# Optimization experiments

Measured on AMD Instinct MI355X. Metric: run time of the kernel, lower is better.

## Reference

```python
import jax, jax.numpy as jnp
import numpy as np
import math

B, T, C = 8, 2048, 1024
H = 16
HD = C // H  # 64 head dim; RoPE operates on HD//2 complex pairs


def setup_inputs() -> dict:
    key = jax.random.key(0)
    k1, k2, k3, k4 = jax.random.split(key, 4)
    x = jax.random.normal(k1, (B, T, C), dtype=jnp.float32)
    # RoPE angles theta[t, i] = t * base**(-2i/HD), as in standard precompute_freqs_cis
    inv_freq = 1.0 / (10000.0 ** (jnp.arange(0, HD, 2, dtype=jnp.float32) / HD))
    freqs = jnp.arange(T, dtype=jnp.float32)[:, None] * inv_freq[None, :]  # [T, HD//2]
    W_attn = jax.random.normal(k2, (C, 3 * C), dtype=jnp.float32) * 0.02
    b_attn = jnp.zeros((3 * C,), dtype=jnp.float32)
    W_proj = jax.random.normal(k3, (C, C), dtype=jnp.float32) * 0.02
    b_proj = jnp.zeros((C,), dtype=jnp.float32)
    return {"x": x, "freqs": freqs, "W_attn": W_attn, "b_attn": b_attn,
            "W_proj": W_proj, "b_proj": b_proj}


def _apply_rope(t, cos, sin):
    # t: [B, T, H, HD] -> view as complex pairs on last dim
    tr = t.reshape(*t.shape[:-1], HD // 2, 2)
    t0, t1 = tr[..., 0], tr[..., 1]
    out0 = t0 * cos - t1 * sin
    out1 = t0 * sin + t1 * cos
    return jnp.stack([out0, out1], axis=-1).reshape(t.shape)


def reference(x, freqs, W_attn, b_attn, W_proj, b_proj):
    Bx, Tx, Cx = x.shape
    qkv = x @ W_attn + b_attn                      # [B, T, 3C]
    q, k, v = jnp.split(qkv, 3, axis=2)
    q = q.reshape(Bx, Tx, H, HD)
    k = k.reshape(Bx, Tx, H, HD)
    v = v.reshape(Bx, Tx, H, HD)
    # rotary embedding (freqs broadcast over batch and heads)
    cos = jnp.cos(freqs)[None, :, None, :]        # [1, T, 1, HD//2]
    sin = jnp.sin(freqs)[None, :, None, :]
    q = _apply_rope(q, cos, sin)
    k = _apply_rope(k, cos, sin)
    # [B, H, T, HD]
    q = q.transpose(0, 2, 1, 3)
    k = k.transpose(0, 2, 1, 3)
    v = v.transpose(0, 2, 1, 3)
    scale = 1.0 / math.sqrt(HD)
    scores = jnp.einsum('bhqd,bhkd->bhqk', q, k) * scale
    causal = jnp.tril(jnp.ones((Tx, Tx), dtype=bool))
    scores = jnp.where(causal[None, None], scores, jnp.finfo(scores.dtype).min)
    att = jax.nn.softmax(scores, axis=-1)
    y = jnp.einsum('bhqk,bhkd->bhqd', att, v)     # [B, H, T, HD]
    y = y.transpose(0, 2, 1, 3).reshape(Bx, Tx, Cx)
    y = y @ W_proj + b_proj
    return y
```

## Files before the change

kernel.cpp:

```cpp
#include <hip/hip_runtime.h>

#define B_ 8
#define T_ 2048
#define C_ 1024
#define H_ 16
#define HD_ 64
#define BH_ (B_ * H_)
#define M_ (B_ * T_)

typedef __attribute__((ext_vector_type(8))) short short8;
typedef __attribute__((ext_vector_type(4))) float floatx4;
typedef __attribute__((ext_vector_type(16))) float floatx16;

__device__ __forceinline__ short f2bf(float f) {
  unsigned int u = __float_as_uint(f);
  u += 0x7fffu + ((u >> 16) & 1u);
  return (short)(u >> 16);
}

__device__ __forceinline__ unsigned cvtpk(float a, float b) {
  unsigned r;
  asm("v_cvt_pk_bf16_f32 %0, %1, %2" : "=v"(r) : "v"(a), "v"(b));
  return r;
}

__device__ __forceinline__ float ex2(float x) {
  float r;
  asm("v_exp_f32 %0, %1" : "=v"(r) : "v"(x));
  return r;
}

__device__ __forceinline__ void g2lds16(const void* g, void* l) {
  __builtin_amdgcn_global_load_lds(
      (const __attribute__((address_space(1))) unsigned int*)g,
      (__attribute__((address_space(3))) unsigned int*)l, 16, 0, 0);
}

__global__ void cvt_x_kernel(const float* __restrict__ x, short* __restrict__ xb, int n8) {
  int i = blockIdx.x * 256 + threadIdx.x;
  if (i >= n8) return;
  const float4* p = reinterpret_cast<const float4*>(x) + (size_t)i * 2;
  float4 a = p[0], b = p[1];
  short8 o;
  o[0] = f2bf(a.x); o[1] = f2bf(a.y); o[2] = f2bf(a.z); o[3] = f2bf(a.w);
  o[4] = f2bf(b.x); o[5] = f2bf(b.y); o[6] = f2bf(b.z); o[7] = f2bf(b.w);
  reinterpret_cast<short8*>(xb)[i] = o;
}

__global__ void transpose_w_kernel(const float* __restrict__ W, short* __restrict__ Wt,
                                   int K, int N) {
  __shared__ float tile[64][65];
  const int k0 = blockIdx.y * 64;
  const int n0 = blockIdx.x * 64;
  const int tid = threadIdx.x;
  const int cc = tid & 15, rr = tid >> 4;
#pragma unroll
  for (int p = 0; p < 4; ++p) {
    int r = p * 16 + rr;
    float4 v = *reinterpret_cast<const float4*>(&W[(size_t)(k0 + r) * N + n0 + cc * 4]);
    tile[r][cc * 4 + 0] = v.x; tile[r][cc * 4 + 1] = v.y;
    tile[r][cc * 4 + 2] = v.z; tile[r][cc * 4 + 3] = v.w;
  }
  __syncthreads();
  const int kk8 = tid & 7, nn = tid >> 3;
#pragma unroll
  for (int p = 0; p < 2; ++p) {
    int n = p * 32 + nn;
    short8 o;
#pragma unroll
    for (int j = 0; j < 8; ++j) o[j] = f2bf(tile[kk8 * 8 + j][n]);
    *reinterpret_cast<short8*>(&Wt[(size_t)(n0 + n) * K + k0 + kk8 * 8]) = o;
  }
}

__global__ void trig_kernel(const float* __restrict__ freqs, float2* __restrict__ cs, int n) {
  int i = blockIdx.x * 256 + threadIdx.x;
  if (i < n) {
    float f = freqs[i];
    cs[i] = make_float2(cosf(f), sinf(f));
  }
}

#define WAIT8 asm volatile("s_waitcnt vmcnt(8)" ::: "memory")
#define WAIT6 asm volatile("s_waitcnt vmcnt(6)" ::: "memory")
#define WAIT4 asm volatile("s_waitcnt vmcnt(4)" ::: "memory")
#define WAIT2 asm volatile("s_waitcnt vmcnt(2)" ::: "memory")
#define WAIT0 asm volatile("s_waitcnt vmcnt(0)" ::: "memory")

#define GITER(T, CUR, NXT)                                                        \
  {                                                                               \
    const int tbR = ((T) & 3) << 15;                                              \
                                     \
    _Pragma("unroll") for (int i = 0; i < 4; ++i)                                 \
        af1[i] = *reinterpret_cast<const short8*>(ldsb + tbR + aoff[4 + i]);      \
    __builtin_amdgcn_s_setprio(1);                                                \
    _Pragma("unroll") for (int m = 0; m < 4; ++m)                                 \
        _Pragma("unroll") for (int n = 0; n < 4; ++n)                             \
            acc[m][n] = __builtin_amdgcn_mfma_f32_16x16x32_bf16(                  \
                af0[m], CUR[n], acc[m][n], 0, 0, 0);                              \
    __builtin_amdgcn_s_setprio(0);                                                \
    \
    if ((T) + 3 < NT) { stageA((T) + 3); stageB((T) + 3); }                       \
    if ((T) < NT - 3) { WAIT8; }                                                  \
    else if ((T) == NT - 3) { WAIT4; }                                            \
    else if ((T) == NT - 2) { WAIT0; }                                            \
    asm volatile("s_waitcnt lgkmcnt(0)" ::: "memory");                            \
    __builtin_amdgcn_s_barrier();                                                 \
    if ((T) + 1 < NT) {                                                           \
      const int tbN = (((T) + 1) & 3) << 15;                                      \
      _Pragma("unroll") for (int n = 0; n < 4; ++n)                               \
          NXT[n] = *reinterpret_cast<const short8*>(ldsb + tbN + boff[n]);        \
      _Pragma("unroll") for (int i = 0; i < 4; ++i)                               \
          af0[i] = *reinterpret_cast<const short8*>(ldsb + tbN + aoff[i]);        \
    }                                                                             \
    __builtin_amdgcn_s_setprio(1);                                                \
    _Pragma("unroll") for (int m = 0; m < 4; ++m)                                 \
        _Pragma("unroll") for (int n = 0; n < 4; ++n)                             \
            acc[4 + m][n] = __builtin_amdgcn_mfma_f32_16x16x32_bf16(              \
                af1[m], CUR[n], acc[4 + m][n], 0, 0, 0);                          \
    __builtin_amdgcn_s_setprio(0);                                                \
  }

template <int EPI>
__global__ __launch_bounds__(512, 2) void gemm8_kernel(
    const short* __restrict__ A, const short* __restrict__ Bt,
    const float* __restrict__ bias, int Ndim, int nbx, float* __restrict__ outF,
    short* __restrict__ Qw, short* __restrict__ Kw, short* __restrict__ Vw,
    const float2* __restrict__ trig) {
  constexpr int Kd = 1024, NT = 32;
  __shared__ short lds[65536];
  const char* ldsb = reinterpret_cast<const char*>(lds);
  const int tid = threadIdx.x, l = tid & 63, w = tid >> 6;
  const int wr = w >> 2, wc = w & 3;

  const int nwg = gridDim.x, qq8 = nwg >> 3;
  const int bid = blockIdx.x;
  const int wg = (bid & 7) * qq8 + (bid >> 3);
  const int npx = nbx >> 2;
  const int p = wg >> 4, q = wg & 15;
  const int bx = (p % npx) * 4 + (q & 3);
  const int by = (p / npx) * 4 + (q >> 2);
  const int m0 = by * 256, n0 = bx * 256;

  const int sup1 = tid >> 3;
  const int lcS = (tid & 7) ^ (sup1 & 7);
  const int rowS = 2 * sup1 + (lcS >> 2);
  const int colS = (lcS & 3) << 3;

  const int cl = l & 15, r4h = l >> 4;
  const int supL = cl >> 1;
  const int aslot = (((cl & 1) << 2) + r4h) ^ supL;
  int aoff[8], boff[4];
#pragma unroll
  for (int m = 0; m < 8; ++m)
    aoff[m] = (wr * 64 + m * 8 + supL) * 128 + aslot * 16;
#pragma unroll
  for (int n = 0; n < 4; ++n)
    boff[n] = 16384 + (wc * 32 + n * 8 + supL) * 128 + aslot * 16;

  auto stageA = [&](int t) {
    const int sb = (t & 3) << 15;
    const int k0 = t * 32;
    g2lds16(&A[(size_t)(m0 + rowS) * Kd + k0 + colS], (char*)lds + sb + tid * 16);
    g2lds16(&A[(size_t)(m0 + rowS + 128) * Kd + k0 + colS],
            (char*)lds + sb + 8192 + tid * 16);
  };
  auto stageB = [&](int t) {
    const int sb = ((t & 3) << 15) + 16384;
    const int k0 = t * 32;
    g2lds16(&Bt[(size_t)(n0 + rowS) * Kd + k0 + colS], (char*)lds + sb + tid * 16);
    g2lds16(&Bt[(size_t)(n0 + rowS + 128) * Kd + k0 + colS],
            (char*)lds + sb + 8192 + tid * 16);
  };

  floatx4 acc[8][4] = {};
  short8 af0[4], af1[4], bbA[4], bbB[4];

  stageA(0); stageB(0);
  stageA(1); stageB(1);
  stageA(2); stageB(2);
  WAIT8;
  __builtin_amdgcn_s_barrier();
#pragma unroll
  for (int n = 0; n < 4; ++n)
    bbA[n] = *reinterpret_cast<const short8*>(ldsb + boff[n]);
#pragma unroll
  for (int i = 0; i < 4; ++i)
    af0[i] = *reinterpret_cast<const short8*>(ldsb + aoff[i]);

  for (int t = 0; t < NT; t += 2) {
    GITER(t, bbA, bbB);
    GITER(t + 1, bbB, bbA);
  }

  const int r4 = r4h * 4;
  if (EPI == 0 && n0 >= 2048) {
    short* vr = &lds[w * 8192];
    const int hh = ((n0 - 2048) >> 6) + wc;
    const int bhv = (m0 >> 11) * 16 + hh;
    const int t0g = (m0 & 2047) + wr * 128;
#pragma unroll
    for (int m = 0; m < 8; ++m) {
#pragma unroll
      for (int n = 0; n < 4; ++n) {
        const int gn = n0 + wc * 64 + n * 16 + cl;
        const float bs = bias[gn];
        const int d = n * 16 + cl;
        const int sW = m * 2 + (r4h >> 1);
        const int byte = d * 256 + (((sW ^ (d & 15))) << 4) + ((r4h & 1) << 3);
        uint2 pv;
        pv.x = cvtpk(acc[m][n][0] + bs, acc[m][n][1] + bs);
        pv.y = cvtpk(acc[m][n][2] + bs, acc[m][n][3] + bs);
        *reinterpret_cast<uint2*>(reinterpret_cast<char*>(vr) + byte) = pv;
      }
    }
#pragma unroll
    for (int g = 0; g < 16; ++g) {
      const int d = g * 4 + r4h;
      const int byte = d * 256 + (((cl ^ (d & 15))) << 4);
      short8 vv = *reinterpret_cast<const short8*>(
          reinterpret_cast<const char*>(vr) + byte);
      *reinterpret_cast<short8*>(&Vw[((size_t)bhv * 64 + d) * 2048 + t0g + cl * 8]) = vv;
    }
  } else {
#pragma unroll
    for (int m = 0; m < 8; ++m) {
#pragma unroll
      for (int n = 0; n < 4; ++n) {
        const int gn = n0 + wc * 64 + n * 16 + cl;
#pragma unroll
        for (int r = 0; r < 4; ++r) {
          const int gm = m0 + wr * 128 + m * 16 + r4 + r;
          float v = acc[m][n][r] + bias[gn];
          if (EPI == 1) {
            outF[(size_t)gm * Ndim + gn] = v;
          } else {
            const int b = gm >> 11, t = gm & 2047;
            const int ccol = gn & 1023;
            const int h = ccol >> 6, d = ccol & 63;
            const int bh = b * 16 + h;
            float2 cs = trig[t * 32 + (d >> 1)];
            float p2 = __shfl_xor(v, 1);
            float o = (d & 1) ? (p2 * cs.y + v * cs.x) : (v * cs.x - p2 * cs.y);
            if ((gn >> 10) == 0) {
              Qw[((size_t)bh * T_ + t) * HD_ + d] = f2bf(o * 0.18033688011112042f);
            } else {
              Kw[((size_t)bh * T_ + t) * HD_ + d] = f2bf(o);
            }
          }
        }
      }
    }
  }
}

__global__ __launch_bounds__(256) void attn_kernel(
    const short* __restrict__ Q, const short* __restrict__ Kw,
    const short* __restrict__ Vt, short* __restrict__ Y) {
  __shared__ short lds[3][8192];
  const int tid = threadIdx.x, l = tid & 63, w = tid >> 6;
  const int ql = l & 31, hi = l >> 5;
  const int bh = blockIdx.x;
  const int qb = 15 - (int)blockIdx.y;
  const int q0w = qb * 128 + w * 32;
  const int jlast = 2 * qb + (w >> 1);
  const int nj = 2 * qb + 2;

  short8 qf[4];
  {
    const size_t qbase = ((size_t)bh * T_ + q0w + ql) * HD_;
#pragma unroll
    for (int s = 0; s < 4; ++s)
      qf[s] = *reinterpret_cast<const short8*>(&Q[qbase + s * 16 + hi * 8]);
  }

  int koffs[4], voffs[4];
#pragma unroll
  for (int s = 0; s < 4; ++s)
    koffs[s] = ql * 64 + (((2 * s + hi) ^ (ql & 7)) * 8);
#pragma unroll
  for (int s2 = 0; s2 < 2; ++s2)
#pragma unroll
    for (int h = 0; h < 2; ++h) {
      int r = 16 * h + (ql >> 1);
      int lc = (ql & 1) * 4 + 2 * s2 + hi;
      voffs[s2 * 2 + h] = r * 64 + ((lc ^ (r & 7)) * 8);
    }

  const int rowSt = tid >> 3, pSt = tid & 7;
  const int gkSt = pSt ^ (rowSt & 7);
  const int dvSt = 2 * rowSt + (gkSt >> 2), kcSt = gkSt & 3;
  const short* kg0 = &Kw[((size_t)bh * T_ + rowSt) * HD_ + gkSt * 8];
  const short* kg1 = &Kw[((size_t)bh * T_ + rowSt + 32) * HD_ + gkSt * 8];
  const short* vg0 = &Vt[((size_t)bh * HD_ + dvSt) * T_ + kcSt * 8];
  const short* vg1 = vg0 + 32;

  floatx16 o0 = {}, o1 = {};
  float l_run = 0.f;

#define STAGE_KV(buf)                                   \
  {                                                     \
    g2lds16(kg0, &lds[buf][0] + tid * 8);               \
    g2lds16(kg1, &lds[buf][2048] + tid * 8);            \
    g2lds16(vg0, &lds[buf][4096] + tid * 8);            \
    g2lds16(vg1, &lds[buf][6144] + tid * 8);            \
    kg0 += 64 * HD_; kg1 += 64 * HD_;                   \
    vg0 += 64; vg1 += 64;                               \
  }

  auto do_half = [&](const short* bK, const short* bV, int koff_add, int vbase,
                     bool domask) {
    floatx16 sx;
#pragma unroll
    for (int r = 0; r < 16; ++r) sx[r] = -16.0f;
#pragma unroll
    for (int s = 0; s < 4; ++s) {
      short8 ka = *reinterpret_cast<const short8*>(bK + koff_add + koffs[s]);
      sx = __builtin_amdgcn_mfma_f32_32x32x16_bf16(ka, qf[s], sx, 0, 0, 0);
    }
    if (domask) {
#pragma unroll
      for (int r = 0; r < 16; ++r) {
        int kb = (r & 3) + 8 * (r >> 2) + 4 * hi;
        if (kb > ql) sx[r] = -1e30f;
      }
    }
#pragma unroll
    for (int r = 0; r < 16; ++r) sx[r] = ex2(sx[r]);
    float a0 = (sx[0] + sx[1]) + (sx[2] + sx[3]);
    float a1 = (sx[4] + sx[5]) + (sx[6] + sx[7]);
    float a2 = (sx[8] + sx[9]) + (sx[10] + sx[11]);
    float a3 = (sx[12] + sx[13]) + (sx[14] + sx[15]);
    l_run += (a0 + a1) + (a2 + a3);
    unsigned pw[8];
#pragma unroll
    for (int i = 0; i < 8; ++i) pw[i] = cvtpk(sx[2 * i], sx[2 * i + 1]);
#pragma unroll
    for (int s2 = 0; s2 < 2; ++s2) {
      unsigned a0w = pw[4 * s2 + 0], a1w = pw[4 * s2 + 1];
      unsigned a2w = pw[4 * s2 + 2], a3w = pw[4 * s2 + 3];
      asm("v_permlane32_swap_b32 %0, %1" : "+v"(a0w), "+v"(a2w));
      asm("v_permlane32_swap_b32 %0, %1" : "+v"(a1w), "+v"(a3w));
      union { unsigned u[4]; short8 s8; } pb;
      pb.u[0] = a0w; pb.u[1] = a1w; pb.u[2] = a2w; pb.u[3] = a3w;
#pragma unroll
      for (int h = 0; h < 2; ++h) {
        short8 va = *reinterpret_cast<const short8*>(bV + vbase + voffs[s2 * 2 + h]);
        if (h == 0) o0 = __builtin_amdgcn_mfma_f32_32x32x16_bf16(va, pb.s8, o0, 0, 0, 0);
        else        o1 = __builtin_amdgcn_mfma_f32_32x32x16_bf16(va, pb.s8, o1, 0, 0, 0);
      }
    }
  };

  STAGE_KV(0);
  STAGE_KV(1);

  for (int j = 0; j < nj; ++j) {
    if (j == nj - 1) { WAIT0; } else { WAIT4; }
    __builtin_amdgcn_s_barrier();
    if (j + 2 < nj) STAGE_KV((j + 2) % 3);

    if (j <= jlast) {
      const short* bK = &lds[j % 3][0];
      const short* bV = &lds[j % 3][4096];
      const bool diag = (j == jlast);
      do_half(bK, bV, 0, 0, diag && ((w & 1) == 0));
      if (!diag || (w & 1))
        do_half(bK, bV, 2048, 2048, diag);
    }
  }

  l_run += __shfl_xor(l_run, 32);
  float inv = 1.0f / l_run;
#pragma unroll
  for (int r = 0; r < 16; ++r) { o0[r] *= inv; o1[r] *= inv; }
  __syncthreads();
  short* tb2 = &lds[0][0] + w * 2048;
#pragma unroll
  for (int h = 0; h < 2; ++h) {
#pragma unroll
    for (int qd = 0; qd < 4; ++qd) {
      int dbase = 32 * h + 8 * qd + 4 * hi;
      uint2 v;
      v.x = h == 0 ? cvtpk(o0[4 * qd], o0[4 * qd + 1]) : cvtpk(o1[4 * qd], o1[4 * qd + 1]);
      v.y = h == 0 ? cvtpk(o0[4 * qd + 2], o0[4 * qd + 3]) : cvtpk(o1[4 * qd + 2], o1[4 * qd + 3]);
      int byte = (ql * 128 + dbase * 2) ^ ((ql & 7) << 4);
      *reinterpret_cast<uint2*>(reinterpret_cast<char*>(tb2) + byte) = v;
    }
  }
  __syncthreads();
  const int bb = bh >> 4, hh = bh & 15;
#pragma unroll
  for (int p = 0; p < 4; ++p) {
    int c = p * 64 + l;
    int q = c >> 3, dc = c & 7;
    int byte = (q * 128 + dc * 16) ^ ((q & 7) << 4);
    short8 v = *reinterpret_cast<const short8*>(reinterpret_cast<const char*>(tb2) + byte);
    *reinterpret_cast<short8*>(
        &Y[((size_t)(bb * T_ + q0w + q)) * C_ + hh * 64 + dc * 8]) = v;
  }
#undef STAGE_KV
}

extern "C" void kernel_launch(void* const* d_in, const int* in_sizes, int n_in,
                              void* d_out, int out_size, void* d_ws, size_t ws_size,
                              hipStream_t stream) {
  const float* x      = (const float*)d_in[0];
  const float* freqs  = (const float*)d_in[1];
  const float* W_attn = (const float*)d_in[2];
  const float* b_attn = (const float*)d_in[3];
  const float* W_proj = (const float*)d_in[4];
  const float* b_proj = (const float*)d_in[5];
  float* out = (float*)d_out;
  char* ws = (char*)d_ws;

  const size_t SZ_QKV = (size_t)BH_ * T_ * HD_ * 2;
  short* Qw  = (short*)(ws);
  short* Kw  = (short*)(ws + SZ_QKV);
  short* Vt  = (short*)(ws + 2 * SZ_QKV);
  short* Xb  = (short*)(ws + 3 * SZ_QKV);
  short* WtA = (short*)(ws + 4 * SZ_QKV);
  short* WtP = (short*)(ws + 4 * SZ_QKV + 6291456);
  float2* trig = (float2*)(ws + 4 * SZ_QKV + 6291456 + 2097152);

  cvt_x_kernel<<<(M_ * C_ / 8 + 255) / 256, 256, 0, stream>>>(x, Xb, M_ * C_ / 8);
  transpose_w_kernel<<<dim3(3 * C_ / 64, C_ / 64), 256, 0, stream>>>(W_attn, WtA, C_, 3 * C_);
  transpose_w_kernel<<<dim3(C_ / 64, C_ / 64), 256, 0, stream>>>(W_proj, WtP, C_, C_);
  trig_kernel<<<(T_ * 32 + 255) / 256, 256, 0, stream>>>(freqs, trig, T_ * 32);

  gemm8_kernel<0><<<dim3((3 * C_ / 256) * (M_ / 256)), 512, 0, stream>>>(
      Xb, WtA, b_attn, 3 * C_, 3 * C_ / 256, nullptr, Qw, Kw, Vt, trig);

  attn_kernel<<<dim3(BH_, 16), 256, 0, stream>>>(Qw, Kw, Vt, Xb);

  gemm8_kernel<1><<<dim3((C_ / 256) * (M_ / 256)), 512, 0, stream>>>(
      Xb, WtP, b_proj, C_, C_ / 256, out, nullptr, nullptr, nullptr, nullptr);
}
```

Before: 270.7 us.

## Split GEMM tiles across 16 waves per workgroup instead of 8

```diff
diff --git a/kernel.cpp b/kernel.cpp
--- a/kernel.cpp
+++ b/kernel.cpp
@@ -91,18 +91,18 @@
   {                                                                               \
     const int tbR = ((T) & 3) << 15;                                              \
                                      \
-    _Pragma("unroll") for (int i = 0; i < 4; ++i)                                 \
-        af1[i] = *reinterpret_cast<const short8*>(ldsb + tbR + aoff[4 + i]);      \
+    af1[0] = *reinterpret_cast<const short8*>(ldsb + tbR + aoff[2]);              \
+    af1[1] = *reinterpret_cast<const short8*>(ldsb + tbR + aoff[3]);              \
     __builtin_amdgcn_s_setprio(1);                                                \
-    _Pragma("unroll") for (int m = 0; m < 4; ++m)                                 \
+    _Pragma("unroll") for (int m = 0; m < 2; ++m)                                 \
         _Pragma("unroll") for (int n = 0; n < 4; ++n)                             \
             acc[m][n] = __builtin_amdgcn_mfma_f32_16x16x32_bf16(                  \
                 af0[m], CUR[n], acc[m][n], 0, 0, 0);                              \
     __builtin_amdgcn_s_setprio(0);                                                \
     \
     if ((T) + 3 < NT) { stageA((T) + 3); stageB((T) + 3); }                       \
-    if ((T) < NT - 3) { WAIT8; }                                                  \
-    else if ((T) == NT - 3) { WAIT4; }                                            \
+    if ((T) < NT - 3) { WAIT4; }                                                  \
+    else if ((T) == NT - 3) { WAIT2; }                                            \
     else if ((T) == NT - 2) { WAIT0; }                                            \
     asm volatile("s_waitcnt lgkmcnt(0)" ::: "memory");                            \
     __builtin_amdgcn_s_barrier();                                                 \
@@ -110,19 +110,19 @@
       const int tbN = (((T) + 1) & 3) << 15;                                      \
       _Pragma("unroll") for (int n = 0; n < 4; ++n)                               \
           NXT[n] = *reinterpret_cast<const short8*>(ldsb + tbN + boff[n]);        \
-      _Pragma("unroll") for (int i = 0; i < 4; ++i)                               \
-          af0[i] = *reinterpret_cast<const short8*>(ldsb + tbN + aoff[i]);        \
+      af0[0] = *reinterpret_cast<const short8*>(ldsb + tbN + aoff[0]);            \
+      af0[1] = *reinterpret_cast<const short8*>(ldsb + tbN + aoff[1]);            \
     }                                                                             \
     __builtin_amdgcn_s_setprio(1);                                                \
-    _Pragma("unroll") for (int m = 0; m < 4; ++m)                                 \
+    _Pragma("unroll") for (int m = 0; m < 2; ++m)                                 \
         _Pragma("unroll") for (int n = 0; n < 4; ++n)                             \
-            acc[4 + m][n] = __builtin_amdgcn_mfma_f32_16x16x32_bf16(              \
-                af1[m], CUR[n], acc[4 + m][n], 0, 0, 0);                          \
+            acc[2 + m][n] = __builtin_amdgcn_mfma_f32_16x16x32_bf16(              \
+                af1[m], CUR[n], acc[2 + m][n], 0, 0, 0);                          \
     __builtin_amdgcn_s_setprio(0);                                                \
   }
 
 template <int EPI>
-__global__ __launch_bounds__(512, 2) void gemm8_kernel(
+__global__ __launch_bounds__(1024, 1) void gemm16_kernel(
     const short* __restrict__ A, const short* __restrict__ Bt,
     const float* __restrict__ bias, int Ndim, int nbx, float* __restrict__ outF,
     short* __restrict__ Qw, short* __restrict__ Kw, short* __restrict__ Vw,
@@ -150,43 +150,36 @@
   const int cl = l & 15, r4h = l >> 4;
   const int supL = cl >> 1;
   const int aslot = (((cl & 1) << 2) + r4h) ^ supL;
-  int aoff[8], boff[4];
-#pragma unroll
-  for (int m = 0; m < 8; ++m)
-    aoff[m] = (wr * 64 + m * 8 + supL) * 128 + aslot * 16;
+  int aoff[4], boff[4];
+#pragma unroll
+  for (int m = 0; m < 4; ++m)
+    aoff[m] = (wr * 32 + m * 8 + supL) * 128 + aslot * 16;
 #pragma unroll
   for (int n = 0; n < 4; ++n)
     boff[n] = 16384 + (wc * 32 + n * 8 + supL) * 128 + aslot * 16;
 
   auto stageA = [&](int t) {
-    const int sb = (t & 3) << 15;
-    const int k0 = t * 32;
-    g2lds16(&A[(size_t)(m0 + rowS) * Kd + k0 + colS], (char*)lds + sb + tid * 16);
-    g2lds16(&A[(size_t)(m0 + rowS + 128) * Kd + k0 + colS],
-            (char*)lds + sb + 8192 + tid * 16);
+    g2lds16(&A[(size_t)(m0 + rowS) * Kd + t * 32 + colS],
+            (char*)lds + ((t & 3) << 15) + tid * 16);
   };
   auto stageB = [&](int t) {
-    const int sb = ((t & 3) << 15) + 16384;
-    const int k0 = t * 32;
-    g2lds16(&Bt[(size_t)(n0 + rowS) * Kd + k0 + colS], (char*)lds + sb + tid * 16);
-    g2lds16(&Bt[(size_t)(n0 + rowS + 128) * Kd + k0 + colS],
-            (char*)lds + sb + 8192 + tid * 16);
+    g2lds16(&Bt[(size_t)(n0 + rowS) * Kd + t * 32 + colS],
+            (char*)lds + ((t & 3) << 15) + 16384 + tid * 16);
   };
 
-  floatx4 acc[8][4] = {};
-  short8 af0[4], af1[4], bbA[4], bbB[4];
+  floatx4 acc[4][4] = {};
+  short8 af0[2], af1[2], bbA[4], bbB[4];
 
   stageA(0); stageB(0);
   stageA(1); stageB(1);
   stageA(2); stageB(2);
-  WAIT8;
+  WAIT4;
   __builtin_amdgcn_s_barrier();
 #pragma unroll
   for (int n = 0; n < 4; ++n)
     bbA[n] = *reinterpret_cast<const short8*>(ldsb + boff[n]);
-#pragma unroll
-  for (int i = 0; i < 4; ++i)
-    af0[i] = *reinterpret_cast<const short8*>(ldsb + aoff[i]);
+  af0[0] = *reinterpret_cast<const short8*>(ldsb + aoff[0]);
+  af0[1] = *reinterpret_cast<const short8*>(ldsb + aoff[1]);
 
   for (int t = 0; t < NT; t += 2) {
     GITER(t, bbA, bbB);
@@ -195,42 +188,43 @@
 
   const int r4 = r4h * 4;
   if (EPI == 0 && n0 >= 2048) {
-    short* vr = &lds[w * 8192];
+    short* vr = &lds[w * 4096];
     const int hh = ((n0 - 2048) >> 6) + wc;
     const int bhv = (m0 >> 11) * 16 + hh;
-    const int t0g = (m0 & 2047) + wr * 128;
-#pragma unroll
-    for (int m = 0; m < 8; ++m) {
+    const int t0g = (m0 & 2047) + wr * 64;
+#pragma unroll
+    for (int m = 0; m < 4; ++m) {
 #pragma unroll
       for (int n = 0; n < 4; ++n) {
         const int gn = n0 + wc * 64 + n * 16 + cl;
         const float bs = bias[gn];
         const int d = n * 16 + cl;
         const int sW = m * 2 + (r4h >> 1);
-        const int byte = d * 256 + (((sW ^ (d & 15))) << 4) + ((r4h & 1) << 3);
+        const int byte = d * 128 + ((sW ^ (d & 7)) << 4) + ((r4h & 1) << 3);
         uint2 pv;
         pv.x = cvtpk(acc[m][n][0] + bs, acc[m][n][1] + bs);
         pv.y = cvtpk(acc[m][n][2] + bs, acc[m][n][3] + bs);
         *reinterpret_cast<uint2*>(reinterpret_cast<char*>(vr) + byte) = pv;
       }
     }
-#pragma unroll
-    for (int g = 0; g < 16; ++g) {
-      const int d = g * 4 + r4h;
-      const int byte = d * 256 + (((cl ^ (d & 15))) << 4);
+    const int d0 = l >> 3, sl = l & 7;
+#pragma unroll
+    for (int g = 0; g < 8; ++g) {
+      const int d = g * 8 + d0;
+      const int byte = d * 128 + ((sl ^ d0) << 4);
       short8 vv = *reinterpret_cast<const short8*>(
           reinterpret_cast<const char*>(vr) + byte);
-      *reinterpret_cast<short8*>(&Vw[((size_t)bhv * 64 + d) * 2048 + t0g + cl * 8]) = vv;
+      *reinterpret_cast<short8*>(&Vw[((size_t)bhv * 64 + d) * 2048 + t0g + sl * 8]) = vv;
     }
   } else {
 #pragma unroll
-    for (int m = 0; m < 8; ++m) {
+    for (int m = 0; m < 4; ++m) {
 #pragma unroll
       for (int n = 0; n < 4; ++n) {
         const int gn = n0 + wc * 64 + n * 16 + cl;
 #pragma unroll
         for (int r = 0; r < 4; ++r) {
-          const int gm = m0 + wr * 128 + m * 16 + r4 + r;
+          const int gm = m0 + wr * 64 + m * 16 + r4 + r;
           float v = acc[m][n][r] + bias[gn];
           if (EPI == 1) {
             outF[(size_t)gm * Ndim + gn] = v;
@@ -428,11 +422,11 @@
   transpose_w_kernel<<<dim3(C_ / 64, C_ / 64), 256, 0, stream>>>(W_proj, WtP, C_, C_);
   trig_kernel<<<(T_ * 32 + 255) / 256, 256, 0, stream>>>(freqs, trig, T_ * 32);
 
-  gemm8_kernel<0><<<dim3((3 * C_ / 256) * (M_ / 256)), 512, 0, stream>>>(
+  gemm16_kernel<0><<<dim3((3 * C_ / 256) * (M_ / 256)), 1024, 0, stream>>>(
       Xb, WtA, b_attn, 3 * C_, 3 * C_ / 256, nullptr, Qw, Kw, Vt, trig);
 
   attn_kernel<<<dim3(BH_, 16), 256, 0, stream>>>(Qw, Kw, Vt, Xb);
 
-  gemm8_kernel<1><<<dim3((C_ / 256) * (M_ / 256)), 512, 0, stream>>>(
+  gemm16_kernel<1><<<dim3((C_ / 256) * (M_ / 256)), 1024, 0, stream>>>(
       Xb, WtP, b_proj, C_, C_ / 256, out, nullptr, nullptr, nullptr, nullptr);
 }
```

Result: slower. 288.3 us (+6.5%).

## Switch GEMM to 4-wave workgroups with larger per-wave output tiles

Applied to the files above, without the earlier changes.

```diff
diff --git a/kernel.cpp b/kernel.cpp
--- a/kernel.cpp
+++ b/kernel.cpp
@@ -81,11 +81,11 @@
   }
 }
 
-#define WAIT8 asm volatile("s_waitcnt vmcnt(8)" ::: "memory")
-#define WAIT6 asm volatile("s_waitcnt vmcnt(6)" ::: "memory")
-#define WAIT4 asm volatile("s_waitcnt vmcnt(4)" ::: "memory")
-#define WAIT2 asm volatile("s_waitcnt vmcnt(2)" ::: "memory")
-#define WAIT0 asm volatile("s_waitcnt vmcnt(0)" ::: "memory")
+#define WAIT16 asm volatile("s_waitcnt vmcnt(16)" ::: "memory")
+#define WAIT8  asm volatile("s_waitcnt vmcnt(8)" ::: "memory")
+#define WAIT4  asm volatile("s_waitcnt vmcnt(4)" ::: "memory")
+#define WAIT2  asm volatile("s_waitcnt vmcnt(2)" ::: "memory")
+#define WAIT0  asm volatile("s_waitcnt vmcnt(0)" ::: "memory")
 
 #define GITER(T, CUR, NXT)                                                        \
   {                                                                               \
@@ -95,34 +95,34 @@
         af1[i] = *reinterpret_cast<const short8*>(ldsb + tbR + aoff[4 + i]);      \
     __builtin_amdgcn_s_setprio(1);                                                \
     _Pragma("unroll") for (int m = 0; m < 4; ++m)                                 \
-        _Pragma("unroll") for (int n = 0; n < 4; ++n)                             \
+        _Pragma("unroll") for (int n = 0; n < 8; ++n)                             \
             acc[m][n] = __builtin_amdgcn_mfma_f32_16x16x32_bf16(                  \
                 af0[m], CUR[n], acc[m][n], 0, 0, 0);                              \
     __builtin_amdgcn_s_setprio(0);                                                \
     \
     if ((T) + 3 < NT) { stageA((T) + 3); stageB((T) + 3); }                       \
-    if ((T) < NT - 3) { WAIT8; }                                                  \
-    else if ((T) == NT - 3) { WAIT4; }                                            \
+    if ((T) < NT - 3) { WAIT16; }                                                 \
+    else if ((T) == NT - 3) { WAIT8; }                                            \
     else if ((T) == NT - 2) { WAIT0; }                                            \
     asm volatile("s_waitcnt lgkmcnt(0)" ::: "memory");                            \
     __builtin_amdgcn_s_barrier();                                                 \
     if ((T) + 1 < NT) {                                                           \
       const int tbN = (((T) + 1) & 3) << 15;                                      \
-      _Pragma("unroll") for (int n = 0; n < 4; ++n)                               \
+      _Pragma("unroll") for (int n = 0; n < 8; ++n)                               \
           NXT[n] = *reinterpret_cast<const short8*>(ldsb + tbN + boff[n]);        \
       _Pragma("unroll") for (int i = 0; i < 4; ++i)                               \
           af0[i] = *reinterpret_cast<const short8*>(ldsb + tbN + aoff[i]);        \
     }                                                                             \
     __builtin_amdgcn_s_setprio(1);                                                \
     _Pragma("unroll") for (int m = 0; m < 4; ++m)                                 \
-        _Pragma("unroll") for (int n = 0; n < 4; ++n)                             \
+        _Pragma("unroll") for (int n = 0; n < 8; ++n)                             \
             acc[4 + m][n] = __builtin_amdgcn_mfma_f32_16x16x32_bf16(              \
                 af1[m], CUR[n], acc[4 + m][n], 0, 0, 0);                          \
     __builtin_amdgcn_s_setprio(0);                                                \
   }
 
 template <int EPI>
-__global__ __launch_bounds__(512, 2) void gemm8_kernel(
+__global__ __launch_bounds__(256, 1) void gemm4_kernel(
     const short* __restrict__ A, const short* __restrict__ Bt,
     const float* __restrict__ bias, int Ndim, int nbx, float* __restrict__ outF,
     short* __restrict__ Qw, short* __restrict__ Kw, short* __restrict__ Vw,
@@ -131,7 +131,7 @@
   __shared__ short lds[65536];
   const char* ldsb = reinterpret_cast<const char*>(lds);
   const int tid = threadIdx.x, l = tid & 63, w = tid >> 6;
-  const int wr = w >> 2, wc = w & 3;
+  const int wr = w >> 1, wc = w & 1;
 
   const int nwg = gridDim.x, qq8 = nwg >> 3;
   const int bid = blockIdx.x;
@@ -142,47 +142,52 @@
   const int by = (p / npx) * 4 + (q >> 2);
   const int m0 = by * 256, n0 = bx * 256;
 
-  const int sup1 = tid >> 3;
-  const int lcS = (tid & 7) ^ (sup1 & 7);
-  const int rowS = 2 * sup1 + (lcS >> 2);
+  const int sup_b = tid >> 3;
+  const int lcS = (tid & 7) ^ (sup_b & 7);
+  const int rowS_b = 2 * sup_b + (lcS >> 2);
   const int colS = (lcS & 3) << 3;
+  const short* aRow[4];
+  const short* bRow[4];
+#pragma unroll
+  for (int i = 0; i < 4; ++i) {
+    aRow[i] = &A[(size_t)(m0 + i * 64 + rowS_b) * Kd + colS];
+    bRow[i] = &Bt[(size_t)(n0 + i * 64 + rowS_b) * Kd + colS];
+  }
 
   const int cl = l & 15, r4h = l >> 4;
   const int supL = cl >> 1;
   const int aslot = (((cl & 1) << 2) + r4h) ^ supL;
-  int aoff[8], boff[4];
+  int aoff[8], boff[8];
 #pragma unroll
   for (int m = 0; m < 8; ++m)
     aoff[m] = (wr * 64 + m * 8 + supL) * 128 + aslot * 16;
 #pragma unroll
-  for (int n = 0; n < 4; ++n)
-    boff[n] = 16384 + (wc * 32 + n * 8 + supL) * 128 + aslot * 16;
+  for (int n = 0; n < 8; ++n)
+    boff[n] = 16384 + (wc * 64 + n * 8 + supL) * 128 + aslot * 16;
 
   auto stageA = [&](int t) {
     const int sb = (t & 3) << 15;
-    const int k0 = t * 32;
-    g2lds16(&A[(size_t)(m0 + rowS) * Kd + k0 + colS], (char*)lds + sb + tid * 16);
-    g2lds16(&A[(size_t)(m0 + rowS + 128) * Kd + k0 + colS],
-            (char*)lds + sb + 8192 + tid * 16);
+#pragma unroll
+    for (int i = 0; i < 4; ++i)
+      g2lds16(aRow[i] + t * 32, (char*)lds + sb + i * 4096 + tid * 16);
   };
   auto stageB = [&](int t) {
     const int sb = ((t & 3) << 15) + 16384;
-    const int k0 = t * 32;
-    g2lds16(&Bt[(size_t)(n0 + rowS) * Kd + k0 + colS], (char*)lds + sb + tid * 16);
-    g2lds16(&Bt[(size_t)(n0 + rowS + 128) * Kd + k0 + colS],
-            (char*)lds + sb + 8192 + tid * 16);
+#pragma unroll
+    for (int i = 0; i < 4; ++i)
+      g2lds16(bRow[i] + t * 32, (char*)lds + sb + i * 4096 + tid * 16);
   };
 
-  floatx4 acc[8][4] = {};
-  short8 af0[4], af1[4], bbA[4], bbB[4];
+  floatx4 acc[8][8] = {};
+  short8 af0[4], af1[4], bbA[8], bbB[8];
 
   stageA(0); stageB(0);
   stageA(1); stageB(1);
   stageA(2); stageB(2);
-  WAIT8;
+  WAIT16;
   __builtin_amdgcn_s_barrier();
 #pragma unroll
-  for (int n = 0; n < 4; ++n)
+  for (int n = 0; n < 8; ++n)
     bbA[n] = *reinterpret_cast<const short8*>(ldsb + boff[n]);
 #pragma unroll
   for (int i = 0; i < 4; ++i)
@@ -196,38 +201,42 @@
   const int r4 = r4h * 4;
   if (EPI == 0 && n0 >= 2048) {
     short* vr = &lds[w * 8192];
-    const int hh = ((n0 - 2048) >> 6) + wc;
-    const int bhv = (m0 >> 11) * 16 + hh;
     const int t0g = (m0 & 2047) + wr * 128;
 #pragma unroll
+    for (int hp = 0; hp < 2; ++hp) {
+      const int hh = ((n0 - 2048) >> 6) + wc * 2 + hp;
+      const int bhv = (m0 >> 11) * 16 + hh;
+#pragma unroll
+      for (int m = 0; m < 8; ++m) {
+#pragma unroll
+        for (int n = 0; n < 4; ++n) {
+          const int gn = n0 + wc * 128 + hp * 64 + n * 16 + cl;
+          const float bs = bias[gn];
+          const int d = n * 16 + cl;
+          const int sW = m * 2 + (r4h >> 1);
+          const int byte = d * 256 + ((sW ^ (d & 15)) << 4) + ((r4h & 1) << 3);
+          uint2 pv;
+          pv.x = cvtpk(acc[m][hp * 4 + n][0] + bs, acc[m][hp * 4 + n][1] + bs);
+          pv.y = cvtpk(acc[m][hp * 4 + n][2] + bs, acc[m][hp * 4 + n][3] + bs);
+          *reinterpret_cast<uint2*>(reinterpret_cast<char*>(vr) + byte) = pv;
+        }
+      }
+#pragma unroll
+      for (int g = 0; g < 16; ++g) {
+        const int d = g * 4 + r4h;
+        const int byte = d * 256 + ((cl ^ (d & 15)) << 4);
+        short8 vv = *reinterpret_cast<const short8*>(
+            reinterpret_cast<const char*>(vr) + byte);
+        *reinterpret_cast<short8*>(
+            &Vw[((size_t)bhv * 64 + d) * 2048 + t0g + cl * 8]) = vv;
+      }
+    }
+  } else {
+#pragma unroll
     for (int m = 0; m < 8; ++m) {
 #pragma unroll
-      for (int n = 0; n < 4; ++n) {
-        const int gn = n0 + wc * 64 + n * 16 + cl;
-        const float bs = bias[gn];
-        const int d = n * 16 + cl;
-        const int sW = m * 2 + (r4h >> 1);
-        const int byte = d * 256 + (((sW ^ (d & 15))) << 4) + ((r4h & 1) << 3);
-        uint2 pv;
-        pv.x = cvtpk(acc[m][n][0] + bs, acc[m][n][1] + bs);
-        pv.y = cvtpk(acc[m][n][2] + bs, acc[m][n][3] + bs);
-        *reinterpret_cast<uint2*>(reinterpret_cast<char*>(vr) + byte) = pv;
-      }
-    }
-#pragma unroll
-    for (int g = 0; g < 16; ++g) {
-      const int d = g * 4 + r4h;
-      const int byte = d * 256 + (((cl ^ (d & 15))) << 4);
-      short8 vv = *reinterpret_cast<const short8*>(
-          reinterpret_cast<const char*>(vr) + byte);
-      *reinterpret_cast<short8*>(&Vw[((size_t)bhv * 64 + d) * 2048 + t0g + cl * 8]) = vv;
-    }
-  } else {
-#pragma unroll
-    for (int m = 0; m < 8; ++m) {
-#pragma unroll
-      for (int n = 0; n < 4; ++n) {
-        const int gn = n0 + wc * 64 + n * 16 + cl;
+      for (int n = 0; n < 8; ++n) {
+        const int gn = n0 + wc * 128 + n * 16 + cl;
 #pragma unroll
         for (int r = 0; r < 4; ++r) {
           const int gm = m0 + wr * 128 + m * 16 + r4 + r;
@@ -428,11 +437,11 @@
   transpose_w_kernel<<<dim3(C_ / 64, C_ / 64), 256, 0, stream>>>(W_proj, WtP, C_, C_);
   trig_kernel<<<(T_ * 32 + 255) / 256, 256, 0, stream>>>(freqs, trig, T_ * 32);
 
-  gemm8_kernel<0><<<dim3((3 * C_ / 256) * (M_ / 256)), 512, 0, stream>>>(
+  gemm4_kernel<0><<<dim3((3 * C_ / 256) * (M_ / 256)), 256, 0, stream>>>(
       Xb, WtA, b_attn, 3 * C_, 3 * C_ / 256, nullptr, Qw, Kw, Vt, trig);
 
   attn_kernel<<<dim3(BH_, 16), 256, 0, stream>>>(Qw, Kw, Vt, Xb);
 
-  gemm8_kernel<1><<<dim3((C_ / 256) * (M_ / 256)), 512, 0, stream>>>(
+  gemm4_kernel<1><<<dim3((C_ / 256) * (M_ / 256)), 256, 0, stream>>>(
       Xb, WtP, b_proj, C_, C_ / 256, out, nullptr, nullptr, nullptr, nullptr);
 }
```

Result: slower. 649.6 us (+140.0%).

## Add dedicated 256x128-tile GEMM kernel for output projection

Applied to the files above, without the earlier changes.

```diff
diff --git a/kernel.cpp b/kernel.cpp
--- a/kernel.cpp
+++ b/kernel.cpp
@@ -84,6 +84,7 @@
 #define WAIT8 asm volatile("s_waitcnt vmcnt(8)" ::: "memory")
 #define WAIT6 asm volatile("s_waitcnt vmcnt(6)" ::: "memory")
 #define WAIT4 asm volatile("s_waitcnt vmcnt(4)" ::: "memory")
+#define WAIT3 asm volatile("s_waitcnt vmcnt(3)" ::: "memory")
 #define WAIT2 asm volatile("s_waitcnt vmcnt(2)" ::: "memory")
 #define WAIT0 asm volatile("s_waitcnt vmcnt(0)" ::: "memory")
 
@@ -121,10 +122,9 @@
     __builtin_amdgcn_s_setprio(0);                                                \
   }
 
-template <int EPI>
 __global__ __launch_bounds__(512, 2) void gemm8_kernel(
     const short* __restrict__ A, const short* __restrict__ Bt,
-    const float* __restrict__ bias, int Ndim, int nbx, float* __restrict__ outF,
+    const float* __restrict__ bias, int Ndim, int nbx,
     short* __restrict__ Qw, short* __restrict__ Kw, short* __restrict__ Vw,
     const float2* __restrict__ trig) {
   constexpr int Kd = 1024, NT = 32;
@@ -194,7 +194,7 @@
   }
 
   const int r4 = r4h * 4;
-  if (EPI == 0 && n0 >= 2048) {
+  if (n0 >= 2048) {
     short* vr = &lds[w * 8192];
     const int hh = ((n0 - 2048) >> 6) + wc;
     const int bhv = (m0 >> 11) * 16 + hh;
@@ -232,23 +232,133 @@
         for (int r = 0; r < 4; ++r) {
           const int gm = m0 + wr * 128 + m * 16 + r4 + r;
           float v = acc[m][n][r] + bias[gn];
-          if (EPI == 1) {
-            outF[(size_t)gm * Ndim + gn] = v;
+          const int b = gm >> 11, t = gm & 2047;
+          const int ccol = gn & 1023;
+          const int h = ccol >> 6, d = ccol & 63;
+          const int bh = b * 16 + h;
+          float2 cs = trig[t * 32 + (d >> 1)];
+          float p2 = __shfl_xor(v, 1);
+          float o = (d & 1) ? (p2 * cs.y + v * cs.x) : (v * cs.x - p2 * cs.y);
+          if ((gn >> 10) == 0) {
+            Qw[((size_t)bh * T_ + t) * HD_ + d] = f2bf(o * 0.18033688011112042f);
           } else {
-            const int b = gm >> 11, t = gm & 2047;
-            const int ccol = gn & 1023;
-            const int h = ccol >> 6, d = ccol & 63;
-            const int bh = b * 16 + h;
-            float2 cs = trig[t * 32 + (d >> 1)];
-            float p2 = __shfl_xor(v, 1);
-            float o = (d & 1) ? (p2 * cs.y + v * cs.x) : (v * cs.x - p2 * cs.y);
-            if ((gn >> 10) == 0) {
-              Qw[((size_t)bh * T_ + t) * HD_ + d] = f2bf(o * 0.18033688011112042f);
-            } else {
-              Kw[((size_t)bh * T_ + t) * HD_ + d] = f2bf(o);
-            }
+            Kw[((size_t)bh * T_ + t) * HD_ + d] = f2bf(o);
           }
         }
+      }
+    }
+  }
+}
+
+__global__ __launch_bounds__(512, 1) void gemm_proj_kernel(
+    const short* __restrict__ A, const short* __restrict__ Bt,
+    const float* __restrict__ bias, float* __restrict__ outF) {
+  constexpr int Kd = 1024, NT = 32, Nd = 1024;
+  __shared__ short lds[49152];
+  const char* ldsb = reinterpret_cast<const char*>(lds);
+  const int tid = threadIdx.x, l = tid & 63, w = tid >> 6;
+  const int wr = w >> 1, wc = w & 1;
+
+  const int nwg = gridDim.x, qq8 = nwg >> 3;
+  const int bid = blockIdx.x;
+  const int wg = (bid & 7) * qq8 + (bid >> 3);
+  const int p = wg >> 4, q = wg & 15;
+  const int bx = (p % 2) * 4 + (q & 3);
+  const int by = (p / 2) * 4 + (q >> 2);
+  const int m0 = by * 256, n0 = bx * 128;
+
+  const int sup1 = tid >> 3;
+  const int lcS = (tid & 7) ^ (sup1 & 7);
+  const int rowS = 2 * sup1 + (lcS >> 2);
+  const int colS = (lcS & 3) << 3;
+
+  const int cl = l & 15, r4h = l >> 4;
+  const int supL = cl >> 1;
+  const int aslot = (((cl & 1) << 2) + r4h) ^ supL;
+  int aoff[4], boff[4];
+#pragma unroll
+  for (int m = 0; m < 4; ++m)
+    aoff[m] = (wr * 32 + m * 8 + supL) * 128 + aslot * 16;
+#pragma unroll
+  for (int n = 0; n < 4; ++n)
+    boff[n] = 16384 + (wc * 32 + n * 8 + supL) * 128 + aslot * 16;
+
+  auto stageA = [&](int t) {
+    const int sb = (t & 3) * 24576;
+    const int k0 = t * 32;
+    g2lds16(&A[(size_t)(m0 + rowS) * Kd + k0 + colS], (char*)lds + sb + tid * 16);
+    g2lds16(&A[(size_t)(m0 + rowS + 128) * Kd + k0 + colS],
+            (char*)lds + sb + 8192 + tid * 16);
+  };
+  auto stageB = [&](int t) {
+    const int sb = (t & 3) * 24576 + 16384;
+    g2lds16(&Bt[(size_t)(n0 + rowS) * Kd + t * 32 + colS],
+            (char*)lds + sb + tid * 16);
+  };
+
+  floatx4 acc[4][4] = {};
+  short8 af0[2], af1[2], bbA[4], bbB[4];
+
+  stageA(0); stageB(0);
+  stageA(1); stageB(1);
+  stageA(2); stageB(2);
+  WAIT6;
+  __builtin_amdgcn_s_barrier();
+#pragma unroll
+  for (int n = 0; n < 4; ++n)
+    bbA[n] = *reinterpret_cast<const short8*>(ldsb + boff[n]);
+  af0[0] = *reinterpret_cast<const short8*>(ldsb + aoff[0]);
+  af0[1] = *reinterpret_cast<const short8*>(ldsb + aoff[1]);
+
+#define PITER(T, CUR, NXT)                                                        \
+  {                                                                               \
+    const int tbR = ((T) & 3) * 24576;                                            \
+    af1[0] = *reinterpret_cast<const short8*>(ldsb + tbR + aoff[2]);              \
+    af1[1] = *reinterpret_cast<const short8*>(ldsb + tbR + aoff[3]);              \
+    __builtin_amdgcn_s_setprio(1);                                                \
+    _Pragma("unroll") for (int m = 0; m < 2; ++m)                                 \
+        _Pragma("unroll") for (int n = 0; n < 4; ++n)                             \
+            acc[m][n] = __builtin_amdgcn_mfma_f32_16x16x32_bf16(                  \
+                af0[m], CUR[n], acc[m][n], 0, 0, 0);                              \
+    __builtin_amdgcn_s_setprio(0);                                                \
+    if ((T) + 3 < NT) { stageA((T) + 3); stageB((T) + 3); }                       \
+    if ((T) < NT - 3) { WAIT6; }                                                  \
+    else if ((T) == NT - 3) { WAIT3; }                                            \
+    else if ((T) == NT - 2) { WAIT0; }                                            \
+    asm volatile("s_waitcnt lgkmcnt(0)" ::: "memory");                            \
+    __builtin_amdgcn_s_barrier();                                                 \
+    if ((T) + 1 < NT) {                                                           \
+      const int tbN = (((T) + 1) & 3) * 24576;                                    \
+      _Pragma("unroll") for (int n = 0; n < 4; ++n)                               \
+          NXT[n] = *reinterpret_cast<const short8*>(ldsb + tbN + boff[n]);        \
+      af0[0] = *reinterpret_cast<const short8*>(ldsb + tbN + aoff[0]);            \
+      af0[1] = *reinterpret_cast<const short8*>(ldsb + tbN + aoff[1]);            \
+    }                                                                             \
+    __builtin_amdgcn_s_setprio(1);                                                \
+    _Pragma("unroll") for (int m = 0; m < 2; ++m)                                 \
+        _Pragma("unroll") for (int n = 0; n < 4; ++n)                             \
+            acc[2 + m][n] = __builtin_amdgcn_mfma_f32_16x16x32_bf16(              \
+                af1[m], CUR[n], acc[2 + m][n], 0, 0, 0);                          \
+    __builtin_amdgcn_s_setprio(0);                                                \
+  }
+
+  for (int t = 0; t < NT; t += 2) {
+    PITER(t, bbA, bbB);
+    PITER(t + 1, bbB, bbA);
+  }
+#undef PITER
+
+  const int r4 = r4h * 4;
+#pragma unroll
+  for (int m = 0; m < 4; ++m) {
+#pragma unroll
+    for (int n = 0; n < 4; ++n) {
+      const int gn = n0 + wc * 64 + n * 16 + cl;
+      const float bs = bias[gn];
+#pragma unroll
+      for (int r = 0; r < 4; ++r) {
+        const int gm = m0 + wr * 64 + m * 16 + r4 + r;
+        outF[(size_t)gm * Nd + gn] = acc[m][n][r] + bs;
       }
     }
   }
@@ -428,11 +538,11 @@
   transpose_w_kernel<<<dim3(C_ / 64, C_ / 64), 256, 0, stream>>>(W_proj, WtP, C_, C_);
   trig_kernel<<<(T_ * 32 + 255) / 256, 256, 0, stream>>>(freqs, trig, T_ * 32);
 
-  gemm8_kernel<0><<<dim3((3 * C_ / 256) * (M_ / 256)), 512, 0, stream>>>(
-      Xb, WtA, b_attn, 3 * C_, 3 * C_ / 256, nullptr, Qw, Kw, Vt, trig);
+  gemm8_kernel<<<dim3((3 * C_ / 256) * (M_ / 256)), 512, 0, stream>>>(
+      Xb, WtA, b_attn, 3 * C_, 3 * C_ / 256, Qw, Kw, Vt, trig);
 
   attn_kernel<<<dim3(BH_, 16), 256, 0, stream>>>(Qw, Kw, Vt, Xb);
 
-  gemm8_kernel<1><<<dim3((C_ / 256) * (M_ / 256)), 512, 0, stream>>>(
-      Xb, WtP, b_proj, C_, C_ / 256, out, nullptr, nullptr, nullptr, nullptr);
-}
+  gemm_proj_kernel<<<dim3((C_ / 128) * (M_ / 256)), 512, 0, stream>>>(
+      Xb, WtP, b_proj, out);
+}
```

New measurement: 275.1 us. No clear change (+1.6%).
